# Kernel tuning notes

Hardware: AMD Instinct MI355X
Metric: run time of the kernel (lower is better)

## Reference

```python
import jax, jax.numpy as jnp
import numpy as np

NSUB = 4  # fixed RK4 substeps per save interval (replaces diffrax adaptive stepping)


def _mlp(x, W0, b0, Wh, bh, Wo, bo, act, fact):
    h = act(W0 @ x + b0)
    for k in range(Wh.shape[0]):  # 3 stacked middle layers (static)
        h = act(Wh[k] @ h + bh[k])
    return fact(Wo @ h + bo)


def _forward(ts, ys, iW0, ib0, iWh, ibh, iWo, ibo, fW0, fb0, fWh, fbh, fWo, fbo, lW, lb):
    hid = iWo.shape[0]
    C = iW0.shape[1]  # in_size + 1 control channels

    def single(yseq):  # yseq: (T, obs)
        tys = jnp.concatenate([ts[:, None], yseq], axis=-1)  # (T, C)
        dts = ts[1:] - ts[:-1]                                # (T-1,)
        diffs = (tys[1:] - tys[:-1]) / dts[:, None]           # (T-1, C)
        # backward Hermite: deriv at t_i is backward difference, forward diff at t_0
        deriv = jnp.concatenate([diffs[:1], diffs], axis=0)   # (T, C)
        d0 = deriv[:-1]
        d1 = deriv[1:]
        c = (3.0 * diffs - 2.0 * d0 - d1) / dts[:, None]
        b = (d0 + d1 - 2.0 * diffs) / (dts * dts)[:, None]

        y0 = _mlp(tys[0], iW0, ib0, iWh, ibh, iWo, ibo, jax.nn.relu, lambda z: z)

        def vf(y):  # (hid, C)
            return _mlp(y, fW0, fb0, fWh, fbh, fWo, fbo, jax.nn.softplus, jnp.tanh).reshape(hid, C)

        def interval(y, xs):
            d0i, ci, bi, h = xs
            hs = h / NSUB

            def xdot(s):  # derivative of cubic Hermite control at local time s
                return d0i + 2.0 * ci * s + 3.0 * bi * s * s

            def f(s, yy):
                return vf(yy) @ xdot(s)

            def sub(k, yy):  # one RK4 substep
                s = k * hs
                k1 = f(s, yy)
                k2 = f(s + hs / 2, yy + hs / 2 * k1)
                k3 = f(s + hs / 2, yy + hs / 2 * k2)
                k4 = f(s + hs, yy + hs * k3)
                return yy + hs / 6 * (k1 + 2 * k2 + 2 * k3 + k4)

            y = jax.lax.fori_loop(0, NSUB, sub, y)
            return y, y

        _, ytail = jax.lax.scan(interval, y0, (d0, c, b, dts))
        ysol = jnp.concatenate([y0[None], ytail], axis=0)  # (T, hid)
        return ysol @ lW.T + lb                            # evolving_out readout

    return jax.vmap(single)(ys)


def setup_inputs() -> dict:
    key = jax.random.key(0)
    ks = jax.random.split(key, 10)
    T, B, obs, hid, width, out_size = 128, 64, 32, 64, 128, 32
    C = obs + 1
    fout = hid * C

    def lin(k, o, i):
        return jax.random.normal(k, (o, i), jnp.float32) / np.sqrt(i).astype(np.float32)

    return {
        "ts": jnp.arange(T, dtype=jnp.float32) / T,
        "ys": jax.random.normal(ks[0], (B, T, obs), jnp.float32) * 0.1,
        "iW0": lin(ks[1], width, C), "ib0": jnp.zeros((width,), jnp.float32),
        "iWh": jax.random.normal(ks[2], (3, width, width), jnp.float32) / np.sqrt(width).astype(np.float32),
        "ibh": jnp.zeros((3, width), jnp.float32),
        "iWo": lin(ks[3], hid, width), "ibo": jnp.zeros((hid,), jnp.float32),
        "fW0": lin(ks[4], width, hid), "fb0": jnp.zeros((width,), jnp.float32),
        "fWh": jax.random.normal(ks[5], (3, width, width), jnp.float32) / np.sqrt(width).astype(np.float32),
        "fbh": jnp.zeros((3, width), jnp.float32),
        "fWo": lin(ks[6], fout, width), "fbo": jnp.zeros((fout,), jnp.float32),
        "lW": lin(ks[7], out_size, hid), "lb": jnp.zeros((out_size,), jnp.float32),
    }


def reference(ts, ys, iW0, ib0, iWh, ibh, iWo, ibo, fW0, fb0, fWh, fbh, fWo, fbo, lW, lb):
    return _forward(ts, ys, iW0, ib0, iWh, ibh, iWo, ibo, fW0, fb0, fWh, fbh, fWo, fbo, lW, lb)
```

## Files before the change

### kernel.cpp

```cpp
#include <hip/hip_runtime.h>
#include <stdint.h>

#define T_N   128
#define B_N   64
#define OBS   32
#define C_N   33
#define HID   64
#define WID   128
#define FOUT  2112
#define OUTD  32
#define NSUB  4
#define NTH   1024

#define NTILE_T  132
#define NPLANES  (NTILE_T*4)
#define WS_NEED  ((size_t)NPLANES * 64 * 16)

typedef __attribute__((ext_vector_type(8))) short  bf16x8;
typedef __attribute__((ext_vector_type(4))) float  f32x4;

__device__ __forceinline__ float b2f(unsigned short u) {
    return __uint_as_float(((unsigned int)u) << 16);
}
__device__ __forceinline__ float b2f_lo(unsigned int u) {
    return __uint_as_float(u << 16);
}
__device__ __forceinline__ float b2f_hi(unsigned int u) {
    return __uint_as_float(u & 0xffff0000u);
}
__device__ __forceinline__ unsigned short f2b(float f) {
    unsigned int u = __float_as_uint(f);
    unsigned int lsb = (u >> 16) & 1u;
    u += 0x7fffu + lsb;
    return (unsigned short)(u >> 16);
}
__device__ __forceinline__ unsigned int pack2(float a, float b) {
    return ((unsigned int)f2b(a)) | (((unsigned int)f2b(b)) << 16);
}
__device__ __forceinline__ unsigned int pkhi(float a, float b) {
    return (__float_as_uint(a) >> 16) | (__float_as_uint(b) & 0xffff0000u);
}
__device__ __forceinline__ unsigned int pklo(float a, float b) {
    float la = a - __uint_as_float(__float_as_uint(a) & 0xffff0000u);
    float lb = b - __uint_as_float(__float_as_uint(b) & 0xffff0000u);
    return pack2(la, lb);
}
__device__ __forceinline__ bf16x8 u4b8(uint4 u) {
    union { uint4 a; bf16x8 b; } x; x.a = u; return x.b;
}
__device__ __forceinline__ float softplus_f(float x) {
    return fmaxf(x, 0.f) + __logf(1.f + __expf(-fabsf(x)));
}
__device__ __forceinline__ float tanh_fast(float x) {
    float e = __expf(2.f * x);
    return 1.f - 2.f / (e + 1.f);
}

struct PolBF16 {
    static __device__ __forceinline__ float ld(const void* p, int i) {
        return b2f(((const unsigned short*)p)[i]);
    }
    static __device__ __forceinline__ void ld8(const void* p, int i, float* o) {
        uint4 u = *(const uint4*)((const unsigned short*)p + i);
        o[0]=b2f_lo(u.x); o[1]=b2f_hi(u.x); o[2]=b2f_lo(u.y); o[3]=b2f_hi(u.y);
        o[4]=b2f_lo(u.z); o[5]=b2f_hi(u.z); o[6]=b2f_lo(u.w); o[7]=b2f_hi(u.w);
    }
    static __device__ __forceinline__ void st(void* p, int i, float v) {
        ((unsigned short*)p)[i] = f2b(v);
    }
};
struct PolF32 {
    static __device__ __forceinline__ float ld(const void* p, int i) {
        return ((const float*)p)[i];
    }
    static __device__ __forceinline__ void ld8(const void* p, int i, float* o) {
        const float4* q = (const float4*)((const float*)p + i);
        float4 a = q[0], b = q[1];
        o[0]=a.x; o[1]=a.y; o[2]=a.z; o[3]=a.w;
        o[4]=b.x; o[5]=b.y; o[6]=b.z; o[7]=b.w;
    }
    static __device__ __forceinline__ void st(void* p, int i, float v) {
        ((float*)p)[i] = v;
    }
};

struct __align__(16) Smem {
    uint4 whv[3][2][NTH];
    uint4 w0v[NTH];
    float rowp[2][FOUT];
    float h[2][WID];
    float y[HID];
    float yt[HID];
    float xd[C_N], d0[C_N], cc[C_N], bb[C_N];
    float fb0[WID];
    float fbh[3][WID];
    float lWt[HID*OUTD];
};

template<class P>
__device__ __forceinline__ void prep_body(const void* fWo, unsigned short* ws) {
    const int e    = blockIdx.x * NTH + threadIdx.x;
    const int p    = e >> 6;
    const int lane = e & 63;
    const int t    = p >> 2;
    const int kb   = p & 3;
    const int row  = 16*t + (lane & 15);
    const int k0   = kb*32 + ((lane >> 4) << 3);
    float v[8];
    P::ld8(fWo, row*WID + k0, v);
    uint4 u;
    u.x = pack2(v[0],v[1]); u.y = pack2(v[2],v[3]);
    u.z = pack2(v[4],v[5]); u.w = pack2(v[6],v[7]);
    ((uint4*)ws)[e] = u;
}
__global__ __launch_bounds__(NTH)
void prep_kernel(const void* ts, const void* fWo, unsigned short* ws) {
    const bool isbf = (((const unsigned short*)ts)[1] == 0x3C00);
    if (isbf) prep_body<PolBF16>(fWo, ws);
    else      prep_body<PolF32>(fWo, ws);
}

template<class P, bool COAL>
__device__ void run_cde(
    const void* ts, const void* ys, const void* iW0, const void* ib0,
    const void* iWh, const void* ibh, const void* iWo, const void* ibo,
    const void* fW0, const void* fb0, const void* fWh, const void* fbh,
    const void* fWo, const void* fbo, const void* lW, const void* lb,
    const void* wWo, void* out, Smem& S)
{
    const int tid  = threadIdx.x;
    const int b    = blockIdx.x;
    const int row8 = tid >> 3;
    const int seg8 = tid & 7;
    const int rot8 = seg8 >> 1;
    const int g16  = tid >> 4;
    const int l16  = tid & 15;
    const int r0   = g16*C_N + l16;
    const int r1   = r0 + 16;
    const int rx   = g16*C_N + 32;
    const int wv   = tid >> 6;
    const int lane = tid & 63;
    const int pr   = wv & 7;
    const int role = wv >> 3;
    const int lg   = lane >> 4;

    {
        const int kb = row8*HID + seg8*8;
        uint4 u;
        u.x = pack2(P::ld(fW0, kb+0), P::ld(fW0, kb+1));
        u.y = pack2(P::ld(fW0, kb+2), P::ld(fW0, kb+3));
        u.z = pack2(P::ld(fW0, kb+4), P::ld(fW0, kb+5));
        u.w = pack2(P::ld(fW0, kb+6), P::ld(fW0, kb+7));
        S.w0v[tid] = u;
    }
    #pragma unroll
    for (int l = 0; l < 3; ++l) {
        #pragma unroll
        for (int c = 0; c < 2; ++c) {
            const int j0 = (c*2 + 0 + rot8) & 3;
            const int j1 = (c*2 + 1 + rot8) & 3;
            const int k0 = (l*WID + row8)*WID + seg8*16 + j0*4;
            const int k1 = (l*WID + row8)*WID + seg8*16 + j1*4;
            uint4 u;
            u.x = pack2(P::ld(fWh, k0+0), P::ld(fWh, k0+1));
            u.y = pack2(P::ld(fWh, k0+2), P::ld(fWh, k0+3));
            u.z = pack2(P::ld(fWh, k1+0), P::ld(fWh, k1+1));
            u.w = pack2(P::ld(fWh, k1+2), P::ld(fWh, k1+3));
            S.whv[l][c][tid] = u;
        }
    }

    const float fb_r0 = P::ld(fbo, r0);
    const float fb_r1 = P::ld(fbo, r1);
    const float fb_rx = P::ld(fbo, rx);

    if (tid < WID)  S.fb0[tid] = P::ld(fb0, tid);
    if (tid < 3*WID) S.fbh[tid>>7][tid&127] = P::ld(fbh, tid);
    for (int i = tid; i < OUTD*HID; i += NTH) {
        int o = i >> 6, kk = i & 63;
        S.lWt[kk*OUTD + o] = P::ld(lW, i);
    }
    if (tid < C_N)
        S.xd[tid] = (tid == 0) ? P::ld(ts, 0) : P::ld(ys, b*T_N*OBS + (tid-1));
    __syncthreads();

    if (tid < WID) {
        float a = P::ld(ib0, tid);
        for (int k2 = 0; k2 < C_N; ++k2) a += P::ld(iW0, tid*C_N + k2) * S.xd[k2];
        S.h[0][tid] = fmaxf(a, 0.f);
    }
    __syncthreads();
    int pp = 0;
    for (int l = 0; l < 3; ++l) {
        if (tid < WID) {
            float a = P::ld(ibh, l*WID + tid);
            for (int k2 = 0; k2 < WID; ++k2)
                a += P::ld(iWh, (l*WID + tid)*WID + k2) * S.h[pp][k2];
            S.h[1-pp][tid] = fmaxf(a, 0.f);
        }
        __syncthreads();
        pp ^= 1;
    }
    if (tid < HID) {
        float a = P::ld(ibo, tid);
        for (int k2 = 0; k2 < WID; ++k2)
            a += P::ld(iWo, tid*WID + k2) * S.h[pp][k2];
        S.y[tid] = a;
    }
    __syncthreads();
    if (tid < OUTD) {
        float a = P::ld(lb, tid);
        for (int k2 = 0; k2 < HID; ++k2) a += S.lWt[k2*OUTD + tid] * S.y[k2];
        P::st(out, b*T_N*OUTD + tid, a);
    }

    #pragma unroll 1
    for (int iv = 0; iv < T_N-1; ++iv) {
        float t0 = P::ld(ts, iv), t1 = P::ld(ts, iv+1);
        float dt = t1 - t0;
        float hs = dt * (1.f/NSUB);
        if (tid < C_N) {
            float v0 = (tid==0) ? t0 : P::ld(ys, b*T_N*OBS + iv*OBS + (tid-1));
            float v1 = (tid==0) ? t1 : P::ld(ys, b*T_N*OBS + (iv+1)*OBS + (tid-1));
            float di = (v1 - v0) / dt;
            float d0v;
            if (iv == 0) d0v = di;
            else {
                float tm = P::ld(ts, iv-1);
                float vm = (tid==0) ? tm : P::ld(ys, b*T_N*OBS + (iv-1)*OBS + (tid-1));
                d0v = (v0 - vm) / (t0 - tm);
            }
            float d1v = di;
            S.d0[tid] = d0v;
            S.cc[tid] = (3.f*di - 2.f*d0v - d1v) / dt;
            S.bb[tid] = (d0v + d1v - 2.f*di) / (dt*dt);
        }
        __syncthreads();

        #pragma unroll 1
        for (int sub = 0; sub < NSUB; ++sub) {
            float s0 = sub * hs;
            float ka = 0.f, kb = 0.f, kc = 0.f;
            #pragma unroll 1
            for (int st = 0; st < 4; ++st) {
                float s = (st==0) ? s0 : ((st==3) ? s0+hs : s0 + 0.5f*hs);
                const float* yin = (st==0) ? S.y : S.yt;

                if (tid < C_N)
                    S.xd[tid] = S.d0[tid] + (2.f*S.cc[tid] + 3.f*S.bb[tid]*s)*s;

                {
                    const float4* y4 = (const float4*)(yin + seg8*8);
                    float4 ya = y4[0], yb = y4[1];
                    uint4 w = S.w0v[tid];
                    float a = b2f_lo(w.x)*ya.x + b2f_hi(w.x)*ya.y
                            + b2f_lo(w.y)*ya.z + b2f_hi(w.y)*ya.w
                            + b2f_lo(w.z)*yb.x + b2f_hi(w.z)*yb.y
                            + b2f_lo(w.w)*yb.z + b2f_hi(w.w)*yb.w;
                    a += __shfl_xor(a, 1);
                    a += __shfl_xor(a, 2);
                    a += __shfl_xor(a, 4);
                    if (seg8 == 0) S.h[0][row8] = softplus_f(a + S.fb0[row8]);
                }
                __syncthreads();

                #pragma unroll
                for (int l = 0; l < 3; ++l) {
                    const int hp = l & 1;
                    const float* hb = S.h[hp] + seg8*16;
                    uint4 wa = S.whv[l][0][tid];
                    uint4 wb = S.whv[l][1][tid];
                    float a;
                    { int j=(0+rot8)&3; float4 hv=*(const float4*)(hb+j*4);
                      a  = b2f_lo(wa.x)*hv.x + b2f_hi(wa.x)*hv.y
                         + b2f_lo(wa.y)*hv.z + b2f_hi(wa.y)*hv.w; }
                    { int j=(1+rot8)&3; float4 hv=*(const float4*)(hb+j*4);
                      a += b2f_lo(wa.z)*hv.x + b2f_hi(wa.z)*hv.y
                         + b2f_lo(wa.w)*hv.z + b2f_hi(wa.w)*hv.w; }
                    { int j=(2+rot8)&3; float4 hv=*(const float4*)(hb+j*4);
                      a += b2f_lo(wb.x)*hv.x + b2f_hi(wb.x)*hv.y
                         + b2f_lo(wb.y)*hv.z + b2f_hi(wb.y)*hv.w; }
                    { int j=(3+rot8)&3; float4 hv=*(const float4*)(hb+j*4);
                      a += b2f_lo(wb.z)*hv.x + b2f_hi(wb.z)*hv.y
                         + b2f_lo(wb.w)*hv.z + b2f_hi(wb.w)*hv.w; }
                    a += __shfl_xor(a, 1);
                    a += __shfl_xor(a, 2);
                    a += __shfl_xor(a, 4);
                    if (seg8 == 0) S.h[1-hp][row8] = softplus_f(a + S.fbh[l][row8]);
                    __syncthreads();
                }

                const float* hin = S.h[1];
                if constexpr (COAL) {
                    const int kbse = role*64 + lg*8;
                    float4 p0 = *(const float4*)(hin + kbse);
                    float4 p1 = *(const float4*)(hin + kbse + 4);
                    float4 p2 = *(const float4*)(hin + kbse + 32);
                    float4 p3 = *(const float4*)(hin + kbse + 36);
                    uint4 bh0, bl0, bh1, bl1;
                    bh0.x=pkhi(p0.x,p0.y); bh0.y=pkhi(p0.z,p0.w);
                    bh0.z=pkhi(p1.x,p1.y); bh0.w=pkhi(p1.z,p1.w);
                    bl0.x=pklo(p0.x,p0.y); bl0.y=pklo(p0.z,p0.w);
                    bl0.z=pklo(p1.x,p1.y); bl0.w=pklo(p1.z,p1.w);
                    bh1.x=pkhi(p2.x,p2.y); bh1.y=pkhi(p2.z,p2.w);
                    bh1.z=pkhi(p3.x,p3.y); bh1.w=pkhi(p3.z,p3.w);
                    bl1.x=pklo(p2.x,p2.y); bl1.y=pklo(p2.z,p2.w);
                    bl1.z=pklo(p3.x,p3.y); bl1.w=pklo(p3.z,p3.w);
                    bf16x8 vh0=u4b8(bh0), vl0=u4b8(bl0);
                    bf16x8 vh1=u4b8(bh1), vl1=u4b8(bl1);

                    const uint4* ap = (const uint4*)wWo
                                    + (pr*4 + 2*role)*64 + lane;
                    const int ntile = (pr < 4) ? 17 : 16;
                    uint4 a0 = ap[0], a1 = ap[64];
                    int t = pr;
                    #pragma unroll 1
                    for (int i = 0; i < ntile; ++i) {
                        uint4 c0 = a0, c1 = a1;
                        if (i + 1 < ntile) {
                            ap += 8*4*64;
                            a0 = ap[0]; a1 = ap[64];
                        }
                        f32x4 acc = {0.f, 0.f, 0.f, 0.f};
                        acc = __builtin_amdgcn_mfma_f32_16x16x32_bf16(
                                  u4b8(c0), vh0, acc, 0, 0, 0);
                        acc = __builtin_amdgcn_mfma_f32_16x16x32_bf16(
                                  u4b8(c0), vl0, acc, 0, 0, 0);
                        acc = __builtin_amdgcn_mfma_f32_16x16x32_bf16(
                                  u4b8(c1), vh1, acc, 0, 0, 0);
                        acc = __builtin_amdgcn_mfma_f32_16x16x32_bf16(
                                  u4b8(c1), vl1, acc, 0, 0, 0);
                        if ((lane & 15) == 0) {
                            float4 st4;
                            st4.x = acc[0]; st4.y = acc[1];
                            st4.z = acc[2]; st4.w = acc[3];
                            *(float4*)&S.rowp[role][16*t + lg*4] = st4;
                        }
                        t += 8;
                    }
                    __syncthreads();

                    {
                        float d0v = S.rowp[0][r0] + S.rowp[1][r0];
                        float d1v = S.rowp[0][r1] + S.rowp[1][r1];
                        float dxv = S.rowp[0][rx] + S.rowp[1][rx];
                        float v0 = tanh_fast(d0v + fb_r0) * S.xd[l16];
                        float v1 = tanh_fast(d1v + fb_r1) * S.xd[16 + l16];
                        float t2 = v0 + v1;
                        t2 += __shfl_xor(t2, 1);
                        t2 += __shfl_xor(t2, 2);
                        t2 += __shfl_xor(t2, 4);
                        t2 += __shfl_xor(t2, 8);
                        float ksum = t2 + tanh_fast(dxv + fb_rx) * S.xd[32];
                        if (l16 == 0) {
                            float yg = S.y[g16];
                            if (st == 0)      { ka = ksum; S.yt[g16] = yg + 0.5f*hs*ksum; }
                            else if (st == 1) { kb = ksum; S.yt[g16] = yg + 0.5f*hs*ksum; }
                            else if (st == 2) { kc = ksum; S.yt[g16] = yg + hs*ksum; }
                            else S.y[g16] = yg + hs*(1.f/6.f)*(ka + 2.f*kb + 2.f*kc + ksum);
                        }
                    }
                } else {
                    float a0 = 0.f, a1 = 0.f, ax = 0.f;
                    #pragma unroll 2
                    for (int j = 0; j < 16; ++j) {
                        const float4* h4 = (const float4*)(hin + j*8);
                        float4 ha = h4[0], hb2 = h4[1];
                        float w8[8];
                        P::ld8(fWo, r0*WID + j*8, w8);
                        a0 += w8[0]*ha.x + w8[1]*ha.y + w8[2]*ha.z + w8[3]*ha.w
                            + w8[4]*hb2.x + w8[5]*hb2.y + w8[6]*hb2.z + w8[7]*hb2.w;
                        P::ld8(fWo, r1*WID + j*8, w8);
                        a1 += w8[0]*ha.x + w8[1]*ha.y + w8[2]*ha.z + w8[3]*ha.w
                            + w8[4]*hb2.x + w8[5]*hb2.y + w8[6]*hb2.z + w8[7]*hb2.w;
                    }
                    {
                        float w8[8];
                        P::ld8(fWo, rx*WID + l16*8, w8);
                        const float4* h4 = (const float4*)(hin + l16*8);
                        float4 ha = h4[0], hb2 = h4[1];
                        ax = w8[0]*ha.x + w8[1]*ha.y + w8[2]*ha.z + w8[3]*ha.w
                           + w8[4]*hb2.x + w8[5]*hb2.y + w8[6]*hb2.z + w8[7]*hb2.w;
                    }
                    ax += __shfl_xor(ax, 1);
                    ax += __shfl_xor(ax, 2);
                    ax += __shfl_xor(ax, 4);
                    ax += __shfl_xor(ax, 8);
                    float v0 = tanh_fast(a0 + fb_r0) * S.xd[l16];
                    float v1 = tanh_fast(a1 + fb_r1) * S.xd[16 + l16];
                    float t2 = v0 + v1;
                    t2 += __shfl_xor(t2, 1);
                    t2 += __shfl_xor(t2, 2);
                    t2 += __shfl_xor(t2, 4);
                    t2 += __shfl_xor(t2, 8);
                    float ksum = t2 + tanh_fast(ax + fb_rx) * S.xd[32];
                    if (l16 == 0) {
                        float yg = S.y[g16];
                        if (st == 0)      { ka = ksum; S.yt[g16] = yg + 0.5f*hs*ksum; }
                        else if (st == 1) { kb = ksum; S.yt[g16] = yg + 0.5f*hs*ksum; }
                        else if (st == 2) { kc = ksum; S.yt[g16] = yg + hs*ksum; }
                        else S.y[g16] = yg + hs*(1.f/6.f)*(ka + 2.f*kb + 2.f*kc + ksum);
                    }
                }
                __syncthreads();
            }
        }

        if (tid < OUTD) {
            float a = P::ld(lb, tid);
            #pragma unroll 8
            for (int k2 = 0; k2 < HID; ++k2) a += S.lWt[k2*OUTD + tid] * S.y[k2];
            P::st(out, b*T_N*OUTD + (iv+1)*OUTD + tid, a);
        }
    }
}

__global__ __launch_bounds__(NTH)
void cde_kernel(const void* ts, const void* ys, const void* iW0, const void* ib0,
                const void* iWh, const void* ibh, const void* iWo, const void* ibo,
                const void* fW0, const void* fb0, const void* fWh, const void* fbh,
                const void* fWo, const void* fbo, const void* lW, const void* lb,
                const unsigned short* ws, int use_ws, void* out)
{
    __shared__ Smem S;
    const bool isbf = (((const unsigned short*)ts)[1] == 0x3C00);
    if (use_ws) {
        if (isbf)
            run_cde<PolBF16, true>(ts, ys, iW0, ib0, iWh, ibh, iWo, ibo,
                                   fW0, fb0, fWh, fbh, fWo, fbo, lW, lb,
                                   ws, out, S);
        else
            run_cde<PolF32, true>(ts, ys, iW0, ib0, iWh, ibh, iWo, ibo,
                                  fW0, fb0, fWh, fbh, fWo, fbo, lW, lb,
                                  ws, out, S);
    } else {
        if (isbf)
            run_cde<PolBF16, false>(ts, ys, iW0, ib0, iWh, ibh, iWo, ibo,
                                    fW0, fb0, fWh, fbh, fWo, fbo, lW, lb,
                                    fWo, out, S);
        else
            run_cde<PolF32, false>(ts, ys, iW0, ib0, iWh, ibh, iWo, ibo,
                                   fW0, fb0, fWh, fbh, fWo, fbo, lW, lb,
                                   fWo, out, S);
    }
}

extern "C" void kernel_launch(void* const* d_in, const int* in_sizes, int n_in,
                              void* d_out, int out_size, void* d_ws, size_t ws_size,
                              hipStream_t stream) {
    (void)in_sizes; (void)n_in; (void)out_size;
    const int use_ws = (ws_size >= WS_NEED) ? 1 : 0;
    if (use_ws) {
        const int nprep = (NPLANES * 64) / NTH;
        hipLaunchKernelGGL(prep_kernel, dim3(nprep), dim3(NTH), 0, stream,
                           d_in[0], d_in[12], (unsigned short*)d_ws);
    }
    hipLaunchKernelGGL(cde_kernel, dim3(B_N), dim3(NTH), 0, stream,
                       d_in[0], d_in[1], d_in[2], d_in[3], d_in[4], d_in[5],
                       d_in[6], d_in[7], d_in[8], d_in[9], d_in[10], d_in[11],
                       d_in[12], d_in[13], d_in[14], d_in[15],
                       (const unsigned short*)d_ws, use_ws, d_out);
}
```

Measured before the change: 13.93 ms.

## Move vector-field MLP hidden layers onto bf16 MFMA with split hi/lo activations

Replaces the scalar dot-product plus shuffle-reduction evaluation of the first and three hidden softplus layers with 16x16x32 bf16 MFMA tiles run by 8 waves. Weights are rearranged in shared memory into MFMA fragment order. Activations are stored once as packed hi/lo bf16 pairs placed in two B columns, then summed with a shuffle, so the output layer no longer repacks them. This aims to cut per-stage ALU and reduction work in the serial RK4 loop. In exchange, half the waves sit idle during the hidden layers, and the non-coalesced path gains an extra unpack step and barrier.

Result: slower. 16.65 ms (+19.6%).

```diff
diff --git a/kernel.cpp b/kernel.cpp
--- a/kernel.cpp
+++ b/kernel.cpp
@@ -85,10 +85,11 @@
 };
 
 struct __align__(16) Smem {
-    uint4 whv[3][2][NTH];
-    uint4 w0v[NTH];
+    uint4 whf[3][32][64];
+    uint4 w0f[16][64];
     float rowp[2][FOUT];
-    float h[2][WID];
+    unsigned int hpk[2][2][64];
+    unsigned int ypk[2][32];
     float y[HID];
     float yt[HID];
     float xd[C_N], d0[C_N], cc[C_N], bb[C_N];
@@ -130,9 +131,6 @@
 {
     const int tid  = threadIdx.x;
     const int b    = blockIdx.x;
-    const int row8 = tid >> 3;
-    const int seg8 = tid & 7;
-    const int rot8 = seg8 >> 1;
     const int g16  = tid >> 4;
     const int l16  = tid & 15;
     const int r0   = g16*C_N + l16;
@@ -140,34 +138,39 @@
     const int rx   = g16*C_N + 32;
     const int wv   = tid >> 6;
     const int lane = tid & 63;
+    const int cidx = lane & 15;
+    const int lg   = lane >> 4;
     const int pr   = wv & 7;
     const int role = wv >> 3;
-    const int lg   = lane >> 4;
 
     {
-        const int kb = row8*HID + seg8*8;
+        const int p = tid >> 6;
+        const int t = p >> 1, kb = p & 1;
+        const int row = 16*t + cidx;
+        const int k0  = kb*32 + lg*8;
         uint4 u;
-        u.x = pack2(P::ld(fW0, kb+0), P::ld(fW0, kb+1));
-        u.y = pack2(P::ld(fW0, kb+2), P::ld(fW0, kb+3));
-        u.z = pack2(P::ld(fW0, kb+4), P::ld(fW0, kb+5));
-        u.w = pack2(P::ld(fW0, kb+6), P::ld(fW0, kb+7));
-        S.w0v[tid] = u;
+        u.x = pack2(P::ld(fW0, row*HID + k0+0), P::ld(fW0, row*HID + k0+1));
+        u.y = pack2(P::ld(fW0, row*HID + k0+2), P::ld(fW0, row*HID + k0+3));
+        u.z = pack2(P::ld(fW0, row*HID + k0+4), P::ld(fW0, row*HID + k0+5));
+        u.w = pack2(P::ld(fW0, row*HID + k0+6), P::ld(fW0, row*HID + k0+7));
+        S.w0f[p][lane] = u;
     }
     #pragma unroll
-    for (int l = 0; l < 3; ++l) {
-        #pragma unroll
-        for (int c = 0; c < 2; ++c) {
-            const int j0 = (c*2 + 0 + rot8) & 3;
-            const int j1 = (c*2 + 1 + rot8) & 3;
-            const int k0 = (l*WID + row8)*WID + seg8*16 + j0*4;
-            const int k1 = (l*WID + row8)*WID + seg8*16 + j1*4;
-            uint4 u;
-            u.x = pack2(P::ld(fWh, k0+0), P::ld(fWh, k0+1));
-            u.y = pack2(P::ld(fWh, k0+2), P::ld(fWh, k0+3));
-            u.z = pack2(P::ld(fWh, k1+0), P::ld(fWh, k1+1));
-            u.w = pack2(P::ld(fWh, k1+2), P::ld(fWh, k1+3));
-            S.whv[l][c][tid] = u;
-        }
+    for (int i = 0; i < 6; ++i) {
+        const int E = i*NTH + tid;
+        const int p = E >> 6;
+        const int ln = E & 63;
+        const int l = p >> 5, rem = p & 31;
+        const int t = rem >> 2, kb = rem & 3;
+        const int row = 16*t + (ln & 15);
+        const int k0  = kb*32 + ((ln >> 4) << 3);
+        const int base = (l*WID + row)*WID + k0;
+        uint4 u;
+        u.x = pack2(P::ld(fWh, base+0), P::ld(fWh, base+1));
+        u.y = pack2(P::ld(fWh, base+2), P::ld(fWh, base+3));
+        u.z = pack2(P::ld(fWh, base+4), P::ld(fWh, base+5));
+        u.w = pack2(P::ld(fWh, base+6), P::ld(fWh, base+7));
+        S.whf[l][rem][ln] = u;
     }
 
     const float fb_r0 = P::ld(fbo, r0);
@@ -187,7 +190,7 @@
     if (tid < WID) {
         float a = P::ld(ib0, tid);
         for (int k2 = 0; k2 < C_N; ++k2) a += P::ld(iW0, tid*C_N + k2) * S.xd[k2];
-        S.h[0][tid] = fmaxf(a, 0.f);
+        S.rowp[0][tid] = fmaxf(a, 0.f);
     }
     __syncthreads();
     int pp = 0;
@@ -195,8 +198,8 @@
         if (tid < WID) {
             float a = P::ld(ibh, l*WID + tid);
             for (int k2 = 0; k2 < WID; ++k2)
-                a += P::ld(iWh, (l*WID + tid)*WID + k2) * S.h[pp][k2];
-            S.h[1-pp][tid] = fmaxf(a, 0.f);
+                a += P::ld(iWh, (l*WID + tid)*WID + k2) * S.rowp[pp][k2];
+            S.rowp[1-pp][tid] = fmaxf(a, 0.f);
         }
         __syncthreads();
         pp ^= 1;
@@ -204,7 +207,7 @@
     if (tid < HID) {
         float a = P::ld(ibo, tid);
         for (int k2 = 0; k2 < WID; ++k2)
-            a += P::ld(iWo, tid*WID + k2) * S.h[pp][k2];
+            a += P::ld(iWo, tid*WID + k2) * S.rowp[pp][k2];
         S.y[tid] = a;
     }
     __syncthreads();
@@ -240,75 +243,98 @@
         #pragma unroll 1
         for (int sub = 0; sub < NSUB; ++sub) {
             float s0 = sub * hs;
-            float ka = 0.f, kb = 0.f, kc = 0.f;
+            float ka = 0.f, kb2 = 0.f, kc = 0.f;
             #pragma unroll 1
             for (int st = 0; st < 4; ++st) {
                 float s = (st==0) ? s0 : ((st==3) ? s0+hs : s0 + 0.5f*hs);
                 const float* yin = (st==0) ? S.y : S.yt;
 
-                if (tid < C_N)
-                    S.xd[tid] = S.d0[tid] + (2.f*S.cc[tid] + 3.f*S.bb[tid]*s)*s;
-
-                {
-                    const float4* y4 = (const float4*)(yin + seg8*8);
-                    float4 ya = y4[0], yb = y4[1];
-                    uint4 w = S.w0v[tid];
-                    float a = b2f_lo(w.x)*ya.x + b2f_hi(w.x)*ya.y
-                            + b2f_lo(w.y)*ya.z + b2f_hi(w.y)*ya.w
-                            + b2f_lo(w.z)*yb.x + b2f_hi(w.z)*yb.y
-                            + b2f_lo(w.w)*yb.z + b2f_hi(w.w)*yb.w;
-                    a += __shfl_xor(a, 1);
-                    a += __shfl_xor(a, 2);
-                    a += __shfl_xor(a, 4);
-                    if (seg8 == 0) S.h[0][row8] = softplus_f(a + S.fb0[row8]);
+                if (tid < 32) {
+                    float v0 = yin[2*tid], v1 = yin[2*tid+1];
+                    S.ypk[0][tid] = pkhi(v0, v1);
+                    S.ypk[1][tid] = pklo(v0, v1);
+                } else if (tid >= 64 && tid < 64 + C_N) {
+                    int c = tid - 64;
+                    S.xd[c] = S.d0[c] + (2.f*S.cc[c] + 3.f*S.bb[c]*s)*s;
                 }
                 __syncthreads();
 
+                if (wv < 8) {
+                    const int t = wv;
+                    const unsigned int* hb = (cidx == 1) ? S.ypk[1] : S.ypk[0];
+                    uint4 b0 = *(const uint4*)(hb + lg*4);
+                    uint4 b1 = *(const uint4*)(hb + 16 + lg*4);
+                    uint4 a0 = S.w0f[t*2+0][lane];
+                    uint4 a1 = S.w0f[t*2+1][lane];
+                    f32x4 acc = {0.f,0.f,0.f,0.f};
+                    acc = __builtin_amdgcn_mfma_f32_16x16x32_bf16(
+                              u4b8(a0), u4b8(b0), acc, 0, 0, 0);
+                    acc = __builtin_amdgcn_mfma_f32_16x16x32_bf16(
+                              u4b8(a1), u4b8(b1), acc, 0, 0, 0);
+                    #pragma unroll
+                    for (int r = 0; r < 4; ++r) acc[r] += __shfl_xor(acc[r], 1);
+                    if (cidx == 0) {
+                        const int rb = 16*t + lg*4;
+                        float h0 = softplus_f(acc[0] + S.fb0[rb+0]);
+                        float h1 = softplus_f(acc[1] + S.fb0[rb+1]);
+                        float h2 = softplus_f(acc[2] + S.fb0[rb+2]);
+                        float h3 = softplus_f(acc[3] + S.fb0[rb+3]);
+                        const int o = 8*t + 2*lg;
+                        S.hpk[0][0][o]   = pkhi(h0,h1);
+                        S.hpk[0][0][o+1] = pkhi(h2,h3);
+                        S.hpk[0][1][o]   = pklo(h0,h1);
+                        S.hpk[0][1][o+1] = pklo(h2,h3);
+                    }
+                }
+                __syncthreads();
+
                 #pragma unroll
                 for (int l = 0; l < 3; ++l) {
-                    const int hp = l & 1;
-                    const float* hb = S.h[hp] + seg8*16;
-                    uint4 wa = S.whv[l][0][tid];
-                    uint4 wb = S.whv[l][1][tid];
-                    float a;
-                    { int j=(0+rot8)&3; float4 hv=*(const float4*)(hb+j*4);
-                      a  = b2f_lo(wa.x)*hv.x + b2f_hi(wa.x)*hv.y
-                         + b2f_lo(wa.y)*hv.z + b2f_hi(wa.y)*hv.w; }
-                    { int j=(1+rot8)&3; float4 hv=*(const float4*)(hb+j*4);
-                      a += b2f_lo(wa.z)*hv.x + b2f_hi(wa.z)*hv.y
-                         + b2f_lo(wa.w)*hv.z + b2f_hi(wa.w)*hv.w; }
-                    { int j=(2+rot8)&3; float4 hv=*(const float4*)(hb+j*4);
-                      a += b2f_lo(wb.x)*hv.x + b2f_hi(wb.x)*hv.y
-                         + b2f_lo(wb.y)*hv.z + b2f_hi(wb.y)*hv.w; }
-                    { int j=(3+rot8)&3; float4 hv=*(const float4*)(hb+j*4);
-                      a += b2f_lo(wb.z)*hv.x + b2f_hi(wb.z)*hv.y
-                         + b2f_lo(wb.w)*hv.z + b2f_hi(wb.w)*hv.w; }
-                    a += __shfl_xor(a, 1);
-                    a += __shfl_xor(a, 2);
-                    a += __shfl_xor(a, 4);
-                    if (seg8 == 0) S.h[1-hp][row8] = softplus_f(a + S.fbh[l][row8]);
+                    if (wv < 8) {
+                        const int t = wv;
+                        const unsigned int* hb = S.hpk[l & 1][(cidx==1) ? 1 : 0];
+                        uint4 b0 = *(const uint4*)(hb + lg*4);
+                        uint4 b1 = *(const uint4*)(hb + 16 + lg*4);
+                        uint4 b2 = *(const uint4*)(hb + 32 + lg*4);
+                        uint4 b3 = *(const uint4*)(hb + 48 + lg*4);
+                        uint4 a0 = S.whf[l][t*4+0][lane];
+                        uint4 a1 = S.whf[l][t*4+1][lane];
+                        uint4 a2 = S.whf[l][t*4+2][lane];
+                        uint4 a3 = S.whf[l][t*4+3][lane];
+                        f32x4 acc = {0.f,0.f,0.f,0.f};
+                        acc = __builtin_amdgcn_mfma_f32_16x16x32_bf16(
+                                  u4b8(a0), u4b8(b0), acc, 0, 0, 0);
+                        acc = __builtin_amdgcn_mfma_f32_16x16x32_bf16(
+                                  u4b8(a1), u4b8(b1), acc, 0, 0, 0);
+                        acc = __builtin_amdgcn_mfma_f32_16x16x32_bf16(
+                                  u4b8(a2), u4b8(b2), acc, 0, 0, 0);
+                        acc = __builtin_amdgcn_mfma_f32_16x16x32_bf16(
+                                  u4b8(a3), u4b8(b3), acc, 0, 0, 0);
+                        #pragma unroll
+                        for (int r = 0; r < 4; ++r) acc[r] += __shfl_xor(acc[r], 1);
+                        if (cidx == 0) {
+                            const int rb = 16*t + lg*4;
+                            float h0 = softplus_f(acc[0] + S.fbh[l][rb+0]);
+                            float h1 = softplus_f(acc[1] + S.fbh[l][rb+1]);
+                            float h2 = softplus_f(acc[2] + S.fbh[l][rb+2]);
+                            float h3 = softplus_f(acc[3] + S.fbh[l][rb+3]);
+                            const int o = 8*t + 2*lg;
+                            unsigned int* dhi = S.hpk[1-(l&1)][0];
+                            unsigned int* dlo = S.hpk[1-(l&1)][1];
+                            dhi[o]   = pkhi(h0,h1);
+                            dhi[o+1] = pkhi(h2,h3);
+                            dlo[o]   = pklo(h0,h1);
+                            dlo[o+1] = pklo(h2,h3);
+                        }
+                    }
                     __syncthreads();
                 }
 
-                const float* hin = S.h[1];
                 if constexpr (COAL) {
-                    const int kbse = role*64 + lg*8;
-                    float4 p0 = *(const float4*)(hin + kbse);
-                    float4 p1 = *(const float4*)(hin + kbse + 4);
-                    float4 p2 = *(const float4*)(hin + kbse + 32);
-                    float4 p3 = *(const float4*)(hin + kbse + 36);
-                    uint4 bh0, bl0, bh1, bl1;
-                    bh0.x=pkhi(p0.x,p0.y); bh0.y=pkhi(p0.z,p0.w);
-                    bh0.z=pkhi(p1.x,p1.y); bh0.w=pkhi(p1.z,p1.w);
-                    bl0.x=pklo(p0.x,p0.y); bl0.y=pklo(p0.z,p0.w);
-                    bl0.z=pklo(p1.x,p1.y); bl0.w=pklo(p1.z,p1.w);
-                    bh1.x=pkhi(p2.x,p2.y); bh1.y=pkhi(p2.z,p2.w);
-                    bh1.z=pkhi(p3.x,p3.y); bh1.w=pkhi(p3.z,p3.w);
-                    bl1.x=pklo(p2.x,p2.y); bl1.y=pklo(p2.z,p2.w);
-                    bl1.z=pklo(p3.x,p3.y); bl1.w=pklo(p3.z,p3.w);
-                    bf16x8 vh0=u4b8(bh0), vl0=u4b8(bl0);
-                    bf16x8 vh1=u4b8(bh1), vl1=u4b8(bl1);
-
+                    const unsigned int* hb = S.hpk[1][(cidx==1) ? 1 : 0];
+                    uint4 b0 = *(const uint4*)(hb + (2*role)*16 + lg*4);
+                    uint4 b1 = *(const uint4*)(hb + (2*role+1)*16 + lg*4);
+                    bf16x8 vb0 = u4b8(b0), vb1 = u4b8(b1);
                     const uint4* ap = (const uint4*)wWo
                                     + (pr*4 + 2*role)*64 + lane;
                     const int ntile = (pr < 4) ? 17 : 16;
@@ -318,19 +344,17 @@
                     for (int i = 0; i < ntile; ++i) {
                         uint4 c0 = a0, c1 = a1;
                         if (i + 1 < ntile) {
-                            ap += 8*4*64;
+                            ap += 2048;
                             a0 = ap[0]; a1 = ap[64];
                         }
-                        f32x4 acc = {0.f, 0.f, 0.f, 0.f};
-                        acc = __builtin_amdgcn_mfma_f32_16x16x32_bf16(
-                                  u4b8(c0), vh0, acc, 0, 0, 0);
-                        acc = __builtin_amdgcn_mfma_f32_16x16x32_bf16(
-                                  u4b8(c0), vl0, acc, 0, 0, 0);
-                        acc = __builtin_amdgcn_mfma_f32_16x16x32_bf16(
-                                  u4b8(c1), vh1, acc, 0, 0, 0);
-                        acc = __builtin_amdgcn_mfma_f32_16x16x32_bf16(
-                                  u4b8(c1), vl1, acc, 0, 0, 0);
-                        if ((lane & 15) == 0) {
+                        f32x4 acc = {0.f,0.f,0.f,0.f};
+                        acc = __builtin_amdgcn_mfma_f32_16x16x32_bf16(
+                                  u4b8(c0), vb0, acc, 0, 0, 0);
+                        acc = __builtin_amdgcn_mfma_f32_16x16x32_bf16(
+                                  u4b8(c1), vb1, acc, 0, 0, 0);
+                        #pragma unroll
+                        for (int r = 0; r < 4; ++r) acc[r] += __shfl_xor(acc[r], 1);
+                        if (cidx == 0) {
                             float4 st4;
                             st4.x = acc[0]; st4.y = acc[1];
                             st4.z = acc[2]; st4.w = acc[3];
@@ -354,13 +378,20 @@
                         float ksum = t2 + tanh_fast(dxv + fb_rx) * S.xd[32];
                         if (l16 == 0) {
                             float yg = S.y[g16];
-                            if (st == 0)      { ka = ksum; S.yt[g16] = yg + 0.5f*hs*ksum; }
-                            else if (st == 1) { kb = ksum; S.yt[g16] = yg + 0.5f*hs*ksum; }
-                            else if (st == 2) { kc = ksum; S.yt[g16] = yg + hs*ksum; }
-                            else S.y[g16] = yg + hs*(1.f/6.f)*(ka + 2.f*kb + 2.f*kc + ksum);
+                            if (st == 0)      { ka = ksum;  S.yt[g16] = yg + 0.5f*hs*ksum; }
+                            else if (st == 1) { kb2 = ksum; S.yt[g16] = yg + 0.5f*hs*ksum; }
+                            else if (st == 2) { kc = ksum;  S.yt[g16] = yg + hs*ksum; }
+                            else S.y[g16] = yg + hs*(1.f/6.f)*(ka + 2.f*kb2 + 2.f*kc + ksum);
                         }
                     }
                 } else {
+                    if (tid < 64) {
+                        unsigned int uh = S.hpk[1][0][tid], ul = S.hpk[1][1][tid];
+                        S.rowp[0][2*tid]   = b2f_lo(uh) + b2f_lo(ul);
+                        S.rowp[0][2*tid+1] = b2f_hi(uh) + b2f_hi(ul);
+                    }
+                    __syncthreads();
+                    const float* hin = S.rowp[0];
                     float a0 = 0.f, a1 = 0.f, ax = 0.f;
                     #pragma unroll 2
                     for (int j = 0; j < 16; ++j) {
@@ -396,10 +427,10 @@
                     float ksum = t2 + tanh_fast(ax + fb_rx) * S.xd[32];
                     if (l16 == 0) {
                         float yg = S.y[g16];
-                        if (st == 0)      { ka = ksum; S.yt[g16] = yg + 0.5f*hs*ksum; }
-                        else if (st == 1) { kb = ksum; S.yt[g16] = yg + 0.5f*hs*ksum; }
-                        else if (st == 2) { kc = ksum; S.yt[g16] = yg + hs*ksum; }
-                        else S.y[g16] = yg + hs*(1.f/6.f)*(ka + 2.f*kb + 2.f*kc + ksum);
+                        if (st == 0)      { ka = ksum;  S.yt[g16] = yg + 0.5f*hs*ksum; }
+                        else if (st == 1) { kb2 = ksum; S.yt[g16] = yg + 0.5f*hs*ksum; }
+                        else if (st == 2) { kc = ksum;  S.yt[g16] = yg + hs*ksum; }
+                        else S.y[g16] = yg + hs*(1.f/6.f)*(ka + 2.f*kb2 + 2.f*kc + ksum);
                     }
                 }
                 __syncthreads();
```
